# Kernel optimization log

Measured on AMD Instinct MI355X. Metric: run time of the kernel, lower is better.

The kernel has to match this reference:

```python
import jax, jax.numpy as jnp
import numpy as np

EPS = 1e-5
ALPHA = 0.05   # propalpha
GDEP = 2       # gcn_depth
LAYERS = 3     # gcn_layers
NUM_TCN = 2    # num_layer tcn units per encoder


def conv1x1(W, b, x):
    # 1x1 Conv2d on [B,C,N,1]: pure channel mix
    return jnp.einsum('oc,bcnl->bonl', W, x) + b[None, :, None, None]


def tcn_unit(Wf, bf, Wg, bg, h):
    # gated TCN unit: tanh(filter) * sigmoid(gate), 1x1 convs (L==1)
    return jnp.tanh(conv1x1(Wf, bf, h)) * jax.nn.sigmoid(conv1x1(Wg, bg, h))


def mixprop(x, A, W, b):
    # MTGNN mixprop: add self-loops, row-normalize, gdep propagation steps,
    # concat hops on channel dim, 1x1 conv mlp. A: [N,N] or [B,N,N].
    N = A.shape[-1]
    A = A + jnp.eye(N, dtype=A.dtype)
    A = A / A.sum(-1, keepdims=True)
    h = x
    outs = [h]
    for _ in range(GDEP):
        if A.ndim == 2:
            hn = jnp.einsum('vw,bcwl->bcvl', A, h)
        else:
            hn = jnp.einsum('bvw,bcwl->bcvl', A, h)
        h = ALPHA * x + (1.0 - ALPHA) * hn
        outs.append(h)
    ho = jnp.concatenate(outs, axis=1)  # [B,(GDEP+1)*C,N,1]
    return conv1x1(W, b, ho)


def layernorm(x, w, b):
    # LayerNorm over (C,N,1) of [B,C,N,1]; idx=arange(N) selects full affine
    mu = x.mean(axis=(1, 2, 3), keepdims=True)
    var = x.var(axis=(1, 2, 3), keepdims=True)
    return (x - mu) / jnp.sqrt(var + EPS) * w[None] + b[None]


def setup_inputs() -> dict:
    key = jax.random.key(0)
    B, N, E, H, S, T = 8, 2048, 32, 128, 256, 12
    ks = jax.random.split(key, 32)
    s = 0.05
    inp = {
        'x': jax.random.normal(ks[0], (B, E, N, 1), jnp.float32),
        'dy_graph': jax.random.uniform(ks[1], (B, N, N), jnp.float32),
        'static_graph': jax.random.uniform(ks[2], (N, N), jnp.float32),
        'spatial_emb': jax.random.normal(ks[3], (B, 32, N, 1), jnp.float32),
        'temporal_d_emb': jax.random.normal(ks[4], (B, 32, N, 1), jnp.float32),
        'temporal_w_emb': jax.random.normal(ks[5], (B, 32, N, 1), jnp.float32),
        'enc_Wf': s * jax.random.normal(ks[6], (LAYERS, NUM_TCN, H, H), jnp.float32),
        'enc_bf': s * jax.random.normal(ks[7], (LAYERS, NUM_TCN, H), jnp.float32),
        'enc_Wg': s * jax.random.normal(ks[8], (LAYERS, NUM_TCN, H, H), jnp.float32),
        'enc_bg': s * jax.random.normal(ks[9], (LAYERS, NUM_TCN, H), jnp.float32),
        'skip_W': s * jax.random.normal(ks[10], (LAYERS, S, H), jnp.float32),
        'skip_b': s * jax.random.normal(ks[11], (LAYERS, S), jnp.float32),
        'norm_w': jnp.ones((LAYERS, E, N, 1), jnp.float32),
        'norm_b': jnp.zeros((LAYERS, E, N, 1), jnp.float32),
        'g0_W': s * jax.random.normal(ks[12], (LAYERS, E, (GDEP + 1) * E), jnp.float32),
        'g0_b': s * jax.random.normal(ks[13], (LAYERS, E), jnp.float32),
        'g1_W': s * jax.random.normal(ks[14], (LAYERS, E, (GDEP + 1) * E), jnp.float32),
        'g1_b': s * jax.random.normal(ks[15], (LAYERS, E), jnp.float32),
        'g2_W': s * jax.random.normal(ks[16], (LAYERS, E, (GDEP + 1) * E), jnp.float32),
        'g2_b': s * jax.random.normal(ks[17], (LAYERS, E), jnp.float32),
        'skipE_W': s * jax.random.normal(ks[18], (S, E), jnp.float32),
        'skipE_b': s * jax.random.normal(ks[19], (S,), jnp.float32),
        'end_W': s * jax.random.normal(ks[20], (T, S), jnp.float32),
        'end_b': s * jax.random.normal(ks[21], (T,), jnp.float32),
    }
    return inp


def reference(x, dy_graph, static_graph, spatial_emb, temporal_d_emb, temporal_w_emb,
              enc_Wf, enc_bf, enc_Wg, enc_bg, skip_W, skip_b, norm_w, norm_b,
              g0_W, g0_b, g1_W, g1_b, g2_W, g2_b, skipE_W, skipE_b, end_W, end_b):
    adp = dy_graph
    skip = 0.0
    for i in range(LAYERS):
        residual = x
        hidden = jnp.concatenate([x, spatial_emb, temporal_d_emb, temporal_w_emb], axis=1)
        for j in range(NUM_TCN):
            hidden = tcn_unit(enc_Wf[i, j], enc_bf[i, j], enc_Wg[i, j], enc_bg[i, j], hidden)
        skip = conv1x1(skip_W[i], skip_b[i], hidden) + skip
        x = (mixprop(x, static_graph, g0_W[i], g0_b[i])
             + mixprop(x, adp, g1_W[i], g1_b[i])
             + mixprop(x, jnp.swapaxes(adp, -1, -2), g2_W[i], g2_b[i]))
        x = x + residual
        x = jax.nn.relu(layernorm(x, norm_w[i], norm_b[i]))
    skip = conv1x1(skipE_W, skipE_b, x) + skip
    return conv1x1(end_W, end_b, skip)  # [B, seq_length, N, 1]
```

## Files before the change

### kernel.cpp

```cpp
#include <hip/hip_runtime.h>
#include <stdint.h>


typedef uint16_t u16;
typedef uint32_t u32;
typedef __attribute__((ext_vector_type(8))) short s8v;
typedef __attribute__((ext_vector_type(4))) float f4v;

#define MFMA16(a,b,c) __builtin_amdgcn_mfma_f32_16x16x32_bf16(a,b,c,0,0,0)

__device__ __forceinline__ float b2f(u16 u){ union{u32 i; float f;} x; x.i=(u32)u<<16; return x.f; }
__device__ __forceinline__ u16 f2b(float f){
  u32 u = __builtin_bit_cast(u32, f);
  u32 r = (u + 0x7fffu + ((u >> 16) & 1u)) >> 16;
  return (u16)r;
}

__global__ __launch_bounds__(256) void kdetect(const u16* __restrict__ x, int* __restrict__ flag)
{
  const int i = threadIdx.x;
  const uint4* p = (const uint4*)x;
  int cnt = 0;
  #pragma unroll
  for (int q = 0; q < 32; q++) {
    const uint4 v = p[i + q*256];
    const u32 w[4] = {v.x, v.y, v.z, v.w};
    #pragma unroll
    for (int e = 0; e < 4; e++) {
      if ((w[e] & 0x7F80u) == 0x7F80u) cnt++;
      if (((w[e] >> 16) & 0x7F80u) == 0x7F80u) cnt++;
    }
  }
  __shared__ int s[256];
  s[i] = cnt; __syncthreads();
  for (int st = 128; st; st >>= 1) { if (i < st) s[i] += s[i+st]; __syncthreads(); }
  if (i == 0) flag[0] = (s[0] > 0) ? 1 : 0;
}

__global__ __launch_bounds__(256) void kcvt4(const void* __restrict__ src, u16* __restrict__ dst,
                                             int n4, const int* __restrict__ flag)
{
  const int i = blockIdx.x*256 + threadIdx.x;
  if (i >= n4) return;
  if (*flag) {
    const float4 v = ((const float4*)src)[i];
    u16 o[4]; o[0]=f2b(v.x); o[1]=f2b(v.y); o[2]=f2b(v.z); o[3]=f2b(v.w);
    *(uint2*)(dst + (long)i*4) = *(uint2*)o;
  } else {
    *(uint2*)(dst + (long)i*4) = ((const uint2*)src)[i];
  }
}

struct CvtTab { const void* s[18]; u16* d[18]; int n4[18]; };
__global__ __launch_bounds__(256) void kcvt_small(CvtTab tb, const int* __restrict__ flag)
{
  const int e = blockIdx.y;
  const int i = blockIdx.x*256 + threadIdx.x;
  if (i >= tb.n4[e]) return;
  if (*flag) {
    const float4 v = ((const float4*)tb.s[e])[i];
    u16 o[4]; o[0]=f2b(v.x); o[1]=f2b(v.y); o[2]=f2b(v.z); o[3]=f2b(v.w);
    *(uint2*)(tb.d[e] + (long)i*4) = *(uint2*)o;
  } else {
    *(uint2*)(tb.d[e] + (long)i*4) = ((const uint2*)tb.s[e])[i];
  }
}

__global__ __launch_bounds__(256) void kcvtT(
    const void* __restrict__ src, u16* __restrict__ dyb, u16* __restrict__ dytb,
    float* __restrict__ rsum, float* __restrict__ csum, const int* __restrict__ flag)
{
  __shared__ u16 tt[256][72];
  const int tid = threadIdx.x;
  const int b = blockIdx.z;
  const long r0 = (long)blockIdx.y*64;
  const long c0 = (long)blockIdx.x*256;
  const int r = tid>>2, cg = (tid&3)*16;
  const long base = (long)b*4194304;
  const int fl = *flag;
  float rs = 0.f;
  #pragma unroll
  for (int st = 0; st < 4; st++) {
    const long cc = c0 + st*64 + cg;
    u16 v16[16];
    if (fl) {
      const float* sp = (const float*)src + base + (r0+r)*2048 + cc;
      #pragma unroll
      for (int q = 0; q < 4; q++) {
        const float4 f = ((const float4*)sp)[q];
        v16[q*4+0]=f2b(f.x); v16[q*4+1]=f2b(f.y); v16[q*4+2]=f2b(f.z); v16[q*4+3]=f2b(f.w);
      }
    } else {
      const u16* sp = (const u16*)src + base + (r0+r)*2048 + cc;
      *(uint4*)&v16[0] = ((const uint4*)sp)[0];
      *(uint4*)&v16[8] = ((const uint4*)sp)[1];
    }
    *(uint4*)(dyb + base + (r0+r)*2048 + cc)     = *(uint4*)&v16[0];
    *(uint4*)(dyb + base + (r0+r)*2048 + cc + 8) = *(uint4*)&v16[8];
    #pragma unroll
    for (int e = 0; e < 16; e++) { rs += b2f(v16[e]); tt[st*64 + cg + e][r] = v16[e]; }
  }
  rs += __shfl_down(rs, 2, 64);
  rs += __shfl_down(rs, 1, 64);
  if ((tid&3)==0) atomicAdd(rsum + b*2048 + r0 + r, rs);
  __syncthreads();
  u16 col[64];
  #pragma unroll
  for (int q = 0; q < 8; q++) *(uint4*)&col[q*8] = *(const uint4*)&tt[tid][q*8];
  float cs = 0.f;
  #pragma unroll
  for (int e = 0; e < 64; e++) cs += b2f(col[e]);
  u16* dp = dytb + base + (c0 + tid)*2048 + r0;
  #pragma unroll
  for (int q = 0; q < 8; q++) *(uint4*)(dp + q*8) = *(uint4*)&col[q*8];
  atomicAdd(csum + b*2048 + c0 + tid, cs);
}

__global__ void kfin(float* __restrict__ v){
  const int i = blockIdx.x*256 + threadIdx.x;
  v[i] = 1.f/(1.f + v[i]);
}

struct P3 {
  const u16* A0; const u16* A1; const u16* A2;
  long ab0, ab1, ab2;
  const u16* X0; const u16* X1; const u16* X2;
  const float* R0; const float* R1; const float* R2;
  long rb0, rb1, rb2;
  u16* O0; u16* O1; u16* O2;
};

template<int SHAREX>
__global__ __launch_bounds__(256) void kprop3(P3 p, long x_bs, long o_bs)
{
  constexpr int NS = SHAREX ? 5 : 9;
  __shared__ f4v red[4][6][64];
  const int tid = threadIdx.x, wave = tid>>6, lane = tid&63;
  const int lw = lane&15, quad = lane>>4;
  const int v0 = blockIdx.x*16;
  const int b = blockIdx.y;
  const long ko = (long)(wave*512 + quad*8);
  const u16* ptr[9];
  ptr[0] = p.A0 + (long)b*p.ab0 + (long)(v0+lw)*2048 + ko;
  ptr[1] = p.A1 + (long)b*p.ab1 + (long)(v0+lw)*2048 + ko;
  ptr[2] = p.A2 + (long)b*p.ab2 + (long)(v0+lw)*2048 + ko;
  ptr[3] = p.X0 + (long)b*x_bs + (long)lw*2048 + ko;
  ptr[4] = p.X0 + (long)b*x_bs + (long)(16+lw)*2048 + ko;
  if (!SHAREX) {
    ptr[5] = p.X1 + (long)b*x_bs + (long)lw*2048 + ko;
    ptr[6] = p.X1 + (long)b*x_bs + (long)(16+lw)*2048 + ko;
    ptr[7] = p.X2 + (long)b*x_bs + (long)lw*2048 + ko;
    ptr[8] = p.X2 + (long)b*x_bs + (long)(16+lw)*2048 + ko;
  }
  f4v acc[6];
  #pragma unroll
  for (int t = 0; t < 6; t++) acc[t] = (f4v){0.f,0.f,0.f,0.f};
  s8v B0[NS][2], B1[NS][2];

  auto LD = [&](s8v (&B)[NS][2], int off){
    #pragma unroll
    for (int s = 0; s < NS; s++) {
      B[s][0] = *(const s8v*)(ptr[s] + off);
      B[s][1] = *(const s8v*)(ptr[s] + off + 32);
    }
  };
  auto FM = [&](s8v (&B)[NS][2]){
    #pragma unroll
    for (int u = 0; u < 2; u++) {
      if (SHAREX) {
        acc[0] = MFMA16(B[0][u], B[3][u], acc[0]);
        acc[1] = MFMA16(B[0][u], B[4][u], acc[1]);
        acc[2] = MFMA16(B[1][u], B[3][u], acc[2]);
        acc[3] = MFMA16(B[1][u], B[4][u], acc[3]);
        acc[4] = MFMA16(B[2][u], B[3][u], acc[4]);
        acc[5] = MFMA16(B[2][u], B[4][u], acc[5]);
      } else {
        acc[0] = MFMA16(B[0][u], B[3][u], acc[0]);
        acc[1] = MFMA16(B[0][u], B[4][u], acc[1]);
        acc[2] = MFMA16(B[1][u], B[5][u], acc[2]);
        acc[3] = MFMA16(B[1][u], B[6][u], acc[3]);
        acc[4] = MFMA16(B[2][u], B[7][u], acc[4]);
        acc[5] = MFMA16(B[2][u], B[8][u], acc[5]);
      }
    }
  };

  LD(B0, 0);
  #pragma unroll 1
  for (int i = 0; i < 3; i++) {
    LD(B1, 64);
    FM(B0);
    LD(B0, 128);
    FM(B1);
    #pragma unroll
    for (int s = 0; s < NS; s++) ptr[s] += 128;
  }
  LD(B1, 64);
  FM(B0);
  FM(B1);

  #pragma unroll
  for (int t = 0; t < 6; t++) red[wave][t][lane] = acc[t];
  __syncthreads();
  if (wave < 3) {
    const int vb = v0 + quad*4;
    const u16* Xg   = (wave==0) ? p.X0 : (wave==1) ? (SHAREX ? p.X0 : p.X1) : (SHAREX ? p.X0 : p.X2);
    const float* Rg = (wave==0) ? p.R0 : (wave==1) ? p.R1 : p.R2;
    const long rbs  = (wave==0) ? p.rb0 : (wave==1) ? p.rb1 : p.rb2;
    u16* Og         = (wave==0) ? p.O0 : (wave==1) ? p.O1 : p.O2;
    #pragma unroll
    for (int nt = 0; nt < 2; nt++) {
      const int t = wave*2 + nt;
      f4v s = red[0][t][lane] + red[1][t][lane] + red[2][t][lane] + red[3][t][lane];
      const int c = nt*16 + lw;
      const u16* dp = Xg + (long)b*x_bs + (long)c*2048 + vb;
      const float* rp = Rg + (long)b*rbs + vb;
      u16 pk[4];
      #pragma unroll
      for (int r = 0; r < 4; r++) pk[r] = f2b((s[r] + b2f(dp[r])) * rp[r]);
      *(uint2*)(Og + (long)b*o_bs + (long)c*2048 + vb) = *(uint2*)pk;
    }
  }
}

template<int TRANSA, int MODE>
__global__ __launch_bounds__(256) void kprop(
    const u16* __restrict__ A, long a_bs, int lda, int K,
    const u16* __restrict__ X, long x_bs, int ldx,
    const u16* __restrict__ D, long d_bs,
    const float* __restrict__ rinv, long r_bs,
    const float* __restrict__ bias,
    u16* __restrict__ out0, float* __restrict__ out1, long o_bs)
{
  __shared__ u16 As[4][2][16][40];
  __shared__ f4v red[4][2][64];
  const int tid = threadIdx.x;
  const int wave = tid >> 6, lane = tid & 63;
  const int lw = lane & 15, quad = lane >> 4;
  const int v0 = blockIdx.x * 16;
  const int ball = blockIdx.z + blockIdx.y;
  const u16* Ab = A + (long)ball * a_bs;
  const u16* Xb = X + (long)ball * x_bs;
  const int KC = K >> 5;

  f4v acc0 = {0.f,0.f,0.f,0.f}, acc1 = {0.f,0.f,0.f,0.f};

  int r0, c0_;
  if (TRANSA == 0) { r0 = lane >> 2; c0_ = (lane & 3) * 8; }
  else             { r0 = lane >> 1; c0_ = (lane & 1) * 8; }

  int ci = wave;
  bool has = ci < KC;
  uint4 d = make_uint4(0,0,0,0);
  if (has) {
    d = (TRANSA == 0)
      ? *(const uint4*)(Ab + (long)(v0 + r0) * lda + ci * 32 + c0_)
      : *(const uint4*)(Ab + (long)(ci * 32 + r0) * lda + v0 + c0_);
  }
  int buf = 0;
  while (has) {
    if (TRANSA == 0) {
      *(uint4*)&As[wave][buf][r0][c0_] = d;
    } else {
      u16 tmp[8]; *(uint4*)tmp = d;
      #pragma unroll
      for (int e = 0; e < 8; e++) As[wave][buf][c0_ + e][r0] = tmp[e];
    }
    const int cn = ci + 4;
    const bool hn = cn < KC;
    if (hn) {
      d = (TRANSA == 0)
        ? *(const uint4*)(Ab + (long)(v0 + r0) * lda + cn * 32 + c0_)
        : *(const uint4*)(Ab + (long)(cn * 32 + r0) * lda + v0 + c0_);
    }
    s8v af = *(const s8v*)&As[wave][buf][lw][quad * 8];
    const u16* xk = Xb + ci * 32 + quad * 8;
    s8v b0 = *(const s8v*)(xk + (long)lw * ldx);
    s8v b1 = *(const s8v*)(xk + (long)(16 + lw) * ldx);
    acc0 = MFMA16(af, b0, acc0);
    acc1 = MFMA16(af, b1, acc1);
    ci = cn; has = hn; buf ^= 1;
  }
  red[wave][0][lane] = acc0;
  red[wave][1][lane] = acc1;
  __syncthreads();
  if (wave == 0) {
    const int vb = v0 + quad * 4;
    #pragma unroll
    for (int nt = 0; nt < 2; nt++) {
      f4v a = red[0][nt][lane] + red[1][nt][lane] + red[2][nt][lane] + red[3][nt][lane];
      const int c = nt * 16 + lw;
      const u16* dp = D + (long)ball * d_bs + (long)c * 2048 + vb;
      if (MODE == 0) {
        const float* rp = rinv + (long)ball * r_bs + vb;
        u16 pk[4];
        #pragma unroll
        for (int r = 0; r < 4; r++) pk[r] = f2b((a[r] + b2f(dp[r])) * rp[r]);
        *(uint2*)(out0 + (long)ball * o_bs + (long)c * 2048 + vb) = *(uint2*)pk;
      } else {
        const float bs = bias[c];
        float4 st;
        st.x = a[0] + bs + b2f(dp[0]);
        st.y = a[1] + bs + b2f(dp[1]);
        st.z = a[2] + bs + b2f(dp[2]);
        st.w = a[3] + bs + b2f(dp[3]);
        *(float4*)(out1 + (long)ball * o_bs + (long)c * 2048 + vb) = st;
      }
    }
  }
}

__global__ __launch_bounds__(256) void ktcn(
    const u16* __restrict__ H, const u16* __restrict__ Wf, const u16* __restrict__ bfv,
    const u16* __restrict__ Wg, const u16* __restrict__ bgv, u16* __restrict__ out)
{
  const int tid = threadIdx.x, wave = tid>>6, lane = tid&63, lw = lane&15, quad = lane>>4;
  const long j0 = (long)blockIdx.x*64 + wave*16;
  const f4v zero = {0.f,0.f,0.f,0.f};
  f4v accf[8], accg[8];
  #pragma unroll
  for (int nt=0; nt<8; nt++){ accf[nt] = zero; accg[nt] = zero; }
  const u16* Arow = H + (j0 + lw)*128 + quad*8;
  #pragma unroll
  for (int k0 = 0; k0 < 128; k0 += 32) {
    s8v a = *(const s8v*)(Arow + k0);
    #pragma unroll
    for (int nt = 0; nt < 8; nt++) {
      const int o = nt*16 + lw;
      s8v bf_ = *(const s8v*)(Wf + o*128 + k0 + quad*8);
      s8v bg_ = *(const s8v*)(Wg + o*128 + k0 + quad*8);
      accf[nt] = MFMA16(a, bf_, accf[nt]);
      accg[nt] = MFMA16(a, bg_, accg[nt]);
    }
  }
  #pragma unroll
  for (int nt = 0; nt < 8; nt++) {
    const int o = nt*16 + lw;
    const float fb = b2f(bfv[o]), gb = b2f(bgv[o]);
    #pragma unroll
    for (int rr = 0; rr < 4; rr++) {
      const long j = j0 + quad*4 + rr;
      const float f = accf[nt][rr] + fb, g = accg[nt][rr] + gb;
      const float e2 = __expf(2.f*f);
      const float th = 1.f - 2.f/(e2 + 1.f);
      const float sg = 1.f/(1.f + __expf(-g));
      out[j*128 + o] = f2b(th*sg);
    }
  }
}

__global__ __launch_bounds__(256) void kskip(
    const u16* __restrict__ A, int lda, int K,
    const u16* __restrict__ W, int ldb,
    const u16* __restrict__ bias,
    float* __restrict__ skipbuf, int addprev, int mode, u16* __restrict__ outb)
{
  const int tid = threadIdx.x, wave = tid>>6, lane = tid&63, lw = lane&15, quad = lane>>4;
  const long j0 = (long)blockIdx.x*64 + wave*16;
  const f4v zero = {0.f,0.f,0.f,0.f};
  f4v acc[16];
  #pragma unroll
  for (int nt=0; nt<16; nt++) acc[nt] = zero;
  const u16* Arow = A + (j0 + lw)*(long)lda + quad*8;
  for (int k0 = 0; k0 < K; k0 += 32) {
    s8v a = *(const s8v*)(Arow + k0);
    #pragma unroll
    for (int nt = 0; nt < 16; nt++) {
      const int o = nt*16 + lw;
      s8v b = *(const s8v*)(W + (long)o*ldb + k0 + quad*8);
      acc[nt] = MFMA16(a, b, acc[nt]);
    }
  }
  #pragma unroll
  for (int nt = 0; nt < 16; nt++) {
    const int o = nt*16 + lw;
    const float bv = b2f(bias[o]);
    #pragma unroll
    for (int rr = 0; rr < 4; rr++) {
      const long j = j0 + quad*4 + rr;
      float v = acc[nt][rr] + bv;
      if (addprev) v += skipbuf[j*256 + o];
      if (mode == 0) skipbuf[j*256 + o] = v;
      else           outb[j*256 + o] = f2b(v);
    }
  }
}

__global__ __launch_bounds__(256) void kend(
    const u16* __restrict__ A, const u16* __restrict__ W, const u16* __restrict__ bias,
    void* __restrict__ outv, const int* __restrict__ flag)
{
  const int tid = threadIdx.x, wave = tid>>6, lane = tid&63, lw = lane&15, quad = lane>>4;
  const long j0 = (long)blockIdx.x*64 + wave*16;
  f4v acc = {0.f,0.f,0.f,0.f};
  const u16* Arow = A + (j0 + lw)*256 + quad*8;
  #pragma unroll
  for (int k0 = 0; k0 < 256; k0 += 32) {
    s8v a = *(const s8v*)(Arow + k0);
    s8v b = {0,0,0,0,0,0,0,0};
    if (lw < 12) b = *(const s8v*)(W + lw*256 + k0 + quad*8);
    acc = MFMA16(a, b, acc);
  }
  if (lw < 12) {
    const float bv = b2f(bias[lw]);
    const int fl = *flag;
    #pragma unroll
    for (int rr = 0; rr < 4; rr++) {
      const long j = j0 + quad*4 + rr;
      const long oi = (j >> 11)*24576 + lw*2048 + (j & 2047);
      const float val = acc[rr] + bv;
      if (fl) ((float*)outv)[oi] = val;
      else    ((u16*)outv)[oi]   = f2b(val);
    }
  }
}

__global__ __launch_bounds__(256) void khid0(
    const void* __restrict__ x, const void* __restrict__ spat,
    const void* __restrict__ tde, const void* __restrict__ twe,
    u16* __restrict__ hid, u16* __restrict__ slot0, const int* __restrict__ flag)
{
  __shared__ u16 t[32][72];
  const int tid = threadIdx.x, b = blockIdx.y, v0 = blockIdx.x*64;
  const int fl = *flag;
  const void* srcs[4] = {x, spat, tde, twe};
  #pragma unroll
  for (int e = 0; e < 4; e++) {
    const int c = tid>>3, v8 = (tid&7)*8;
    const long boff = (long)c*2048 + v0 + v8;
    u16 o8[8];
    if (fl) {
      const float* sp = (const float*)srcs[e] + (long)b*65536 + boff;
      const float4 a = ((const float4*)sp)[0], bb = ((const float4*)sp)[1];
      o8[0]=f2b(a.x); o8[1]=f2b(a.y); o8[2]=f2b(a.z); o8[3]=f2b(a.w);
      o8[4]=f2b(bb.x); o8[5]=f2b(bb.y); o8[6]=f2b(bb.z); o8[7]=f2b(bb.w);
    } else {
      *(uint4*)o8 = *(const uint4*)((const u16*)srcs[e] + (long)b*65536 + boff);
    }
    if (e == 0) *(uint4*)(slot0 + (long)b*458752 + boff) = *(uint4*)o8;
    *(uint4*)&t[c][v8] = *(uint4*)o8;
    __syncthreads();
    const int jl = tid>>2, c8 = (tid&3)*8;
    u16 q8[8];
    #pragma unroll
    for (int i = 0; i < 8; i++) q8[i] = t[c8 + i][jl];
    *(uint4*)(hid + ((long)b*2048 + v0 + jl)*128 + e*32 + c8) = *(uint4*)q8;
    __syncthreads();
  }
}

__global__ __launch_bounds__(256) void krowsum(const u16* __restrict__ src, float* __restrict__ outv, int nrows)
{
  const int wave = threadIdx.x>>6, lane = threadIdx.x&63;
  const int row = blockIdx.x*4 + wave;
  if (row >= nrows) return;
  const u16* p = src + (long)row*2048 + lane*8;
  float s = 0.f;
  #pragma unroll
  for (int it = 0; it < 4; it++) {
    u16 v[8]; *(uint4*)v = *(const uint4*)(p + it*512);
    #pragma unroll
    for (int e = 0; e < 8; e++) s += b2f(v[e]);
  }
  #pragma unroll
  for (int off = 32; off; off >>= 1) s += __shfl_down(s, off, 64);
  if (lane == 0) outv[row] = 1.f/(1.f + s);
}

__global__ __launch_bounds__(256) void kweff(
    const u16* __restrict__ g0W, const u16* __restrict__ g1W, const u16* __restrict__ g2W,
    const u16* __restrict__ g0b, const u16* __restrict__ g1b, const u16* __restrict__ g2b,
    int ioff, int boff, u16* __restrict__ weff, float* __restrict__ bw)
{
  const int idx = blockIdx.x*256 + threadIdx.x;
  if (idx < 32) bw[idx] = b2f(g0b[boff+idx]) + b2f(g1b[boff+idx]) + b2f(g2b[boff+idx]);
  if (idx >= 7168) return;
  const int o = idx / 224, m = idx % 224;
  const u16* Ws[3] = {g0W + ioff, g1W + ioff, g2W + ioff};
  float val;
  if (m < 32) {
    val = 0.f;
    #pragma unroll
    for (int g = 0; g < 3; g++) {
      const float w0 = b2f(Ws[g][o*96 + m]);
      const float w1 = b2f(Ws[g][o*96 + 32 + m]);
      const float w2 = b2f(Ws[g][o*96 + 64 + m]);
      val += w0 + 0.05f*(w1 + w2);
    }
  } else {
    const int f = (m - 32) >> 5, cc = m & 31;
    const int g = f >> 1, typ = f & 1;
    const float w1 = b2f(Ws[g][o*96 + 32 + cc]);
    const float w2 = b2f(Ws[g][o*96 + 64 + cc]);
    val = (typ == 0) ? (0.95f*w1 + 0.0475f*w2) : (0.9025f*w2);
  }
  weff[o*224 + m] = f2b(val);
}

__global__ __launch_bounds__(256) void kstats(const float* __restrict__ xpre, float* __restrict__ raw)
{
  const int b = blockIdx.y, tid = threadIdx.x;
  const float4* p = (const float4*)(xpre + (long)b*65536 + (long)blockIdx.x*8192);
  float s = 0.f, q = 0.f;
  #pragma unroll
  for (int i = 0; i < 8; i++) {
    const float4 v = p[tid + i*256];
    s += v.x + v.y + v.z + v.w;
    q += v.x*v.x + v.y*v.y + v.z*v.z + v.w*v.w;
  }
  __shared__ float ss[256], qq[256];
  ss[tid] = s; qq[tid] = q;
  __syncthreads();
  for (int st = 128; st; st >>= 1) {
    if (tid < st) { ss[tid] += ss[tid+st]; qq[tid] += qq[tid+st]; }
    __syncthreads();
  }
  if (tid == 0) { atomicAdd(raw + b*2, ss[0]); atomicAdd(raw + b*2 + 1, qq[0]); }
}

__global__ __launch_bounds__(256) void kapply(
    const float* __restrict__ xpre, const float* __restrict__ raw,
    const u16* __restrict__ nw, const u16* __restrict__ nb,
    u16* __restrict__ slot0, u16* __restrict__ hid)
{
  __shared__ u16 t[32][72];
  const int tid = threadIdx.x, b = blockIdx.y, v0 = blockIdx.x*64;
  const float mu = raw[b*2] * (1.f/65536.f);
  const float var = raw[b*2+1] * (1.f/65536.f) - mu*mu;
  const float rs = rsqrtf(var + 1e-5f);
  const int c = tid>>3, v8 = (tid&7)*8;
  const long boff = (long)c*2048 + v0 + v8;
  float4 xa = *(const float4*)(xpre + (long)b*65536 + boff);
  float4 xbv = *(const float4*)(xpre + (long)b*65536 + boff + 4);
  u16 wv[8], bv[8], o8[8];
  *(uint4*)wv = *(const uint4*)(nw + boff);
  *(uint4*)bv = *(const uint4*)(nb + boff);
  const float xs[8] = {xa.x, xa.y, xa.z, xa.w, xbv.x, xbv.y, xbv.z, xbv.w};
  #pragma unroll
  for (int e = 0; e < 8; e++) {
    float y = (xs[e] - mu) * rs * b2f(wv[e]) + b2f(bv[e]);
    y = fmaxf(y, 0.f);
    o8[e] = f2b(y);
    t[c][v8 + e] = o8[e];
  }
  *(uint4*)(slot0 + (long)b*458752 + boff) = *(uint4*)o8;
  __syncthreads();
  const int jl = tid>>2, c8 = (tid&3)*8;
  u16 q8[8];
  #pragma unroll
  for (int e = 0; e < 8; e++) q8[e] = t[c8 + e][jl];
  *(uint4*)(hid + ((long)b*2048 + v0 + jl)*128 + c8) = *(uint4*)q8;
}

extern "C" void kernel_launch(void* const* d_in, const int* in_sizes, int n_in,
                              void* d_out, int out_size, void* d_ws, size_t ws_size,
                              hipStream_t stream)
{
  (void)in_sizes; (void)n_in; (void)out_size; (void)ws_size;

  char* ws = (char*)d_ws;
  u16*   pbuf = (u16*)(ws + 0);
  u16*   hid  = (u16*)(ws + 7340032);
  u16*   hb1  = (u16*)(ws + 11534336);
  u16*   hb2  = (u16*)(ws + 15728640);
  float* skip = (float*)(ws + 19922944);
  u16*   xsb  = (u16*)(ws + 36700160);
  float* xpre = (float*)(ws + 45088768);
  u16*   weff = (u16*)(ws + 47185920);
  float* bw   = (float*)(ws + 47202304);
  float* rst  = (float*)(ws + 47203328);
  float* rdy  = (float*)(ws + 47211520);
  float* cdy  = (float*)(ws + 47277056);
  int*   flag = (int*)(ws + 47343616);
  float* raw  = (float*)(ws + 47343744);

  size_t coff = 50331648;
  auto alloc = [&](size_t elems) -> u16* {
    u16* p = (u16*)(ws + coff);
    coff += ((elems*2 + 255)/256)*256;
    return p;
  };
  u16* dyb   = alloc(33554432);
  u16* stgb  = alloc(4194304);
  u16* encWf = alloc(98304);
  u16* encbf = alloc(768);
  u16* encWg = alloc(98304);
  u16* encbg = alloc(768);
  u16* skW   = alloc(98304);
  u16* skb   = alloc(768);
  u16* nw    = alloc(196608);
  u16* nb    = alloc(196608);
  u16* g0W   = alloc(9216);
  u16* g0b   = alloc(96);
  u16* g1W   = alloc(9216);
  u16* g1b   = alloc(96);
  u16* g2W   = alloc(9216);
  u16* g2b   = alloc(96);
  u16* sEW   = alloc(8192);
  u16* sEb   = alloc(256);
  u16* eW    = alloc(3072);
  u16* eb    = alloc(12);
  u16* dytb  = alloc(33554432);

  hipLaunchKernelGGL(kdetect, dim3(1), dim3(256), 0, stream, (const u16*)d_in[0], flag);

  CvtTab tb;
  {
    const void* ss[18] = { d_in[6], d_in[7], d_in[8], d_in[9], d_in[10], d_in[11],
      d_in[12], d_in[13], d_in[14], d_in[15], d_in[16], d_in[17], d_in[18], d_in[19],
      d_in[20], d_in[21], d_in[22], d_in[23] };
    u16* dd[18] = { encWf, encbf, encWg, encbg, skW, skb, nw, nb,
      g0W, g0b, g1W, g1b, g2W, g2b, sEW, sEb, eW, eb };
    const int nn[18] = { 24576, 192, 24576, 192, 24576, 192, 49152, 49152,
      2304, 24, 2304, 24, 2304, 24, 2048, 64, 768, 3 };
    for (int e = 0; e < 18; e++) { tb.s[e] = ss[e]; tb.d[e] = dd[e]; tb.n4[e] = nn[e]; }
  }
  hipLaunchKernelGGL(kcvt_small, dim3(192, 18), dim3(256), 0, stream, tb, flag);
  hipLaunchKernelGGL(kcvt4, dim3(4096), dim3(256), 0, stream, d_in[2], stgb, 1048576, flag);

  hipMemsetAsync(rdy, 0, 131072, stream);
  hipMemsetAsync(raw, 0, 192, stream);
  hipLaunchKernelGGL(kcvtT, dim3(8,32,8), dim3(256), 0, stream,
      d_in[1], dyb, dytb, rdy, cdy, flag);
  hipLaunchKernelGGL(kfin, dim3(128), dim3(256), 0, stream, rdy);
  hipLaunchKernelGGL(krowsum, dim3(512), dim3(256), 0, stream, stgb, rst, 2048);
  hipLaunchKernelGGL(khid0, dim3(32,8), dim3(256), 0, stream,
      d_in[0], d_in[3], d_in[4], d_in[5], hid, pbuf, flag);

  const long PB = 458752;
  const long SL = 65536;
  const long DYB = 4194304;

  for (int i = 0; i < 3; i++) {
    hipLaunchKernelGGL(ktcn, dim3(256), dim3(256), 0, stream,
        hid, encWf + (i*2+0)*16384, encbf + (i*2+0)*128, encWg + (i*2+0)*16384, encbg + (i*2+0)*128, hb1);
    hipLaunchKernelGGL(ktcn, dim3(256), dim3(256), 0, stream,
        hb1, encWf + (i*2+1)*16384, encbf + (i*2+1)*128, encWg + (i*2+1)*16384, encbg + (i*2+1)*128, hb2);
    hipLaunchKernelGGL(kskip, dim3(256), dim3(256), 0, stream,
        hb2, 128, 128, skW + i*32768, 128, skb + i*256, skip, (i>0)?1:0, 0, (u16*)nullptr);
    hipLaunchKernelGGL(kweff, dim3(28), dim3(256), 0, stream,
        g0W, g1W, g2W, g0b, g1b, g2b, i*3072, i*32, weff, bw);

    P3 p1;
    p1.A0 = stgb; p1.A1 = dyb; p1.A2 = dytb;
    p1.ab0 = 0;   p1.ab1 = DYB; p1.ab2 = DYB;
    p1.X0 = pbuf; p1.X1 = pbuf; p1.X2 = pbuf;
    p1.R0 = rst;  p1.R1 = rdy;  p1.R2 = cdy;
    p1.rb0 = 0;   p1.rb1 = 2048; p1.rb2 = 2048;
    p1.O0 = pbuf + 1*SL; p1.O1 = pbuf + 3*SL; p1.O2 = pbuf + 5*SL;
    hipLaunchKernelGGL((kprop3<1>), dim3(128,8), dim3(256), 0, stream, p1, PB, PB);

    P3 p2 = p1;
    p2.X0 = pbuf + 1*SL; p2.X1 = pbuf + 3*SL; p2.X2 = pbuf + 5*SL;
    p2.O0 = pbuf + 2*SL; p2.O1 = pbuf + 4*SL; p2.O2 = pbuf + 6*SL;
    hipLaunchKernelGGL((kprop3<0>), dim3(128,8), dim3(256), 0, stream, p2, PB, PB);

    hipLaunchKernelGGL((kprop<1,1>), dim3(128,1,8), dim3(256), 0, stream,
        pbuf, PB, 2048, 224, weff, 0L, 224, pbuf, PB, (const float*)nullptr, 0L, bw, (u16*)nullptr, xpre, 65536L);
    hipLaunchKernelGGL(kstats, dim3(8,8), dim3(256), 0, stream, xpre, raw + i*16);
    hipLaunchKernelGGL(kapply, dim3(32,8), dim3(256), 0, stream,
        xpre, raw + i*16, nw + i*65536, nb + i*65536, pbuf, hid);
  }
  hipLaunchKernelGGL(kskip, dim3(256), dim3(256), 0, stream,
      hid, 128, 32, sEW, 32, sEb, skip, 1, 1, xsb);
  hipLaunchKernelGGL(kend, dim3(256), dim3(256), 0, stream, xsb, eW, eb, d_out, flag);
}
```

Baseline: 893.6 us.

## Fuse TCN chain, mixprop combine, final convs and preprocessing kernels

Merges the two gated TCN units and the skip conv into one kernel that keeps intermediates in shared memory. Propagation kernels now also write a transposed hop buffer, so a new combine kernel can do the effective-weight GEMM and the layernorm statistics in one pass. The reciprocal row-sum finalisation moves into the propagation epilogue, and the static-graph conversion is fused with its row sum. The skipE and end convs become one kernel, and the effective weights are precomputed once for all layers. This cuts launches and global round trips, but adds scattered transposed stores and more shared memory per block.

Result: slower. 937.9 us (+5.0%).

```diff
diff --git a/kernel.cpp b/kernel.cpp
--- a/kernel.cpp
+++ b/kernel.cpp
@@ -8,6 +8,11 @@
 typedef __attribute__((ext_vector_type(4))) float f4v;
 
 #define MFMA16(a,b,c) __builtin_amdgcn_mfma_f32_16x16x32_bf16(a,b,c,0,0,0)
+
+constexpr long PB  = 262144;
+constexpr long SL  = 65536;
+constexpr long TB  = 393216;
+constexpr long DYB = 4194304;
 
 __device__ __forceinline__ float b2f(u16 u){ union{u32 i; float f;} x; x.i=(u32)u<<16; return x.f; }
 __device__ __forceinline__ u16 f2b(float f){
@@ -35,20 +40,6 @@
   s[i] = cnt; __syncthreads();
   for (int st = 128; st; st >>= 1) { if (i < st) s[i] += s[i+st]; __syncthreads(); }
   if (i == 0) flag[0] = (s[0] > 0) ? 1 : 0;
-}
-
-__global__ __launch_bounds__(256) void kcvt4(const void* __restrict__ src, u16* __restrict__ dst,
-                                             int n4, const int* __restrict__ flag)
-{
-  const int i = blockIdx.x*256 + threadIdx.x;
-  if (i >= n4) return;
-  if (*flag) {
-    const float4 v = ((const float4*)src)[i];
-    u16 o[4]; o[0]=f2b(v.x); o[1]=f2b(v.y); o[2]=f2b(v.z); o[3]=f2b(v.w);
-    *(uint2*)(dst + (long)i*4) = *(uint2*)o;
-  } else {
-    *(uint2*)(dst + (long)i*4) = ((const uint2*)src)[i];
-  }
 }
 
 struct CvtTab { const void* s[18]; u16* d[18]; int n4[18]; };
@@ -66,71 +57,103 @@
   }
 }
 
+__global__ __launch_bounds__(256) void kstg(
+    const void* __restrict__ src, u16* __restrict__ dst, float* __restrict__ rst,
+    const int* __restrict__ flag)
+{
+  const int wave = threadIdx.x>>6, lane = threadIdx.x&63;
+  const int row = blockIdx.x*4 + wave;
+  const int fl = *flag;
+  float s = 0.f;
+  #pragma unroll
+  for (int q = 0; q < 8; q++) {
+    const long off = (long)row*2048 + q*256 + lane*4;
+    u16 v4[4];
+    if (fl) {
+      const float4 f = *(const float4*)((const float*)src + off);
+      v4[0]=f2b(f.x); v4[1]=f2b(f.y); v4[2]=f2b(f.z); v4[3]=f2b(f.w);
+    } else {
+      *(uint2*)v4 = *(const uint2*)((const u16*)src + off);
+    }
+    *(uint2*)(dst + off) = *(uint2*)v4;
+    #pragma unroll
+    for (int e = 0; e < 4; e++) s += b2f(v4[e]);
+  }
+  #pragma unroll
+  for (int off = 32; off; off >>= 1) s += __shfl_down(s, off, 64);
+  if (lane == 0) rst[row] = s;
+}
+
 __global__ __launch_bounds__(256) void kcvtT(
     const void* __restrict__ src, u16* __restrict__ dyb, u16* __restrict__ dytb,
     float* __restrict__ rsum, float* __restrict__ csum, const int* __restrict__ flag)
 {
-  __shared__ u16 tt[256][72];
+  __shared__ u32 tt[256][34];
   const int tid = threadIdx.x;
   const int b = blockIdx.z;
-  const long r0 = (long)blockIdx.y*64;
-  const long c0 = (long)blockIdx.x*256;
-  const int r = tid>>2, cg = (tid&3)*16;
+  const long r0 = (long)blockIdx.y*64, c0 = (long)blockIdx.x*256;
+  const int rp = tid>>3, c4 = (tid&7)*4;
   const long base = (long)b*4194304;
   const int fl = *flag;
-  float rs = 0.f;
-  #pragma unroll
-  for (int st = 0; st < 4; st++) {
-    const long cc = c0 + st*64 + cg;
-    u16 v16[16];
+  float rs0 = 0.f, rs1 = 0.f;
+  #pragma unroll
+  for (int j = 0; j < 8; j++) {
+    const long cc = c0 + c4 + 32*j;
+    u16 v0_[4], v1_[4];
     if (fl) {
-      const float* sp = (const float*)src + base + (r0+r)*2048 + cc;
-      #pragma unroll
-      for (int q = 0; q < 4; q++) {
-        const float4 f = ((const float4*)sp)[q];
-        v16[q*4+0]=f2b(f.x); v16[q*4+1]=f2b(f.y); v16[q*4+2]=f2b(f.z); v16[q*4+3]=f2b(f.w);
-      }
+      const float* s0 = (const float*)src + base + (r0 + 2*rp)*2048 + cc;
+      const float4 f0 = *(const float4*)s0;
+      const float4 f1 = *(const float4*)(s0 + 2048);
+      v0_[0]=f2b(f0.x); v0_[1]=f2b(f0.y); v0_[2]=f2b(f0.z); v0_[3]=f2b(f0.w);
+      v1_[0]=f2b(f1.x); v1_[1]=f2b(f1.y); v1_[2]=f2b(f1.z); v1_[3]=f2b(f1.w);
     } else {
-      const u16* sp = (const u16*)src + base + (r0+r)*2048 + cc;
-      *(uint4*)&v16[0] = ((const uint4*)sp)[0];
-      *(uint4*)&v16[8] = ((const uint4*)sp)[1];
-    }
-    *(uint4*)(dyb + base + (r0+r)*2048 + cc)     = *(uint4*)&v16[0];
-    *(uint4*)(dyb + base + (r0+r)*2048 + cc + 8) = *(uint4*)&v16[8];
-    #pragma unroll
-    for (int e = 0; e < 16; e++) { rs += b2f(v16[e]); tt[st*64 + cg + e][r] = v16[e]; }
-  }
-  rs += __shfl_down(rs, 2, 64);
-  rs += __shfl_down(rs, 1, 64);
-  if ((tid&3)==0) atomicAdd(rsum + b*2048 + r0 + r, rs);
+      const u16* s0 = (const u16*)src + base + (r0 + 2*rp)*2048 + cc;
+      *(uint2*)v0_ = *(const uint2*)s0;
+      *(uint2*)v1_ = *(const uint2*)(s0 + 2048);
+    }
+    *(uint2*)(dyb + base + (r0+2*rp)*2048 + cc)   = *(uint2*)v0_;
+    *(uint2*)(dyb + base + (r0+2*rp+1)*2048 + cc) = *(uint2*)v1_;
+    #pragma unroll
+    for (int e = 0; e < 4; e++) {
+      rs0 += b2f(v0_[e]); rs1 += b2f(v1_[e]);
+      tt[c4 + 32*j + e][rp] = (u32)v0_[e] | ((u32)v1_[e] << 16);
+    }
+  }
+  rs0 += __shfl_down(rs0, 4, 8); rs0 += __shfl_down(rs0, 2, 8); rs0 += __shfl_down(rs0, 1, 8);
+  rs1 += __shfl_down(rs1, 4, 8); rs1 += __shfl_down(rs1, 2, 8); rs1 += __shfl_down(rs1, 1, 8);
+  if ((tid & 7) == 0) {
+    atomicAdd(rsum + b*2048 + r0 + 2*rp, rs0);
+    atomicAdd(rsum + b*2048 + r0 + 2*rp + 1, rs1);
+  }
   __syncthreads();
-  u16 col[64];
-  #pragma unroll
-  for (int q = 0; q < 8; q++) *(uint4*)&col[q*8] = *(const uint4*)&tt[tid][q*8];
-  float cs = 0.f;
-  #pragma unroll
-  for (int e = 0; e < 64; e++) cs += b2f(col[e]);
+  u32 cw[32];
+  #pragma unroll
+  for (int q = 0; q < 16; q++) {
+    const uint2 w2 = *(const uint2*)&tt[tid][q*2];
+    cw[q*2] = w2.x; cw[q*2+1] = w2.y;
+  }
+  u16 col[64]; float cs = 0.f;
+  #pragma unroll
+  for (int rr = 0; rr < 32; rr++) {
+    col[2*rr]   = (u16)(cw[rr] & 0xffffu);
+    col[2*rr+1] = (u16)(cw[rr] >> 16);
+    cs += b2f(col[2*rr]) + b2f(col[2*rr+1]);
+  }
   u16* dp = dytb + base + (c0 + tid)*2048 + r0;
   #pragma unroll
   for (int q = 0; q < 8; q++) *(uint4*)(dp + q*8) = *(uint4*)&col[q*8];
   atomicAdd(csum + b*2048 + c0 + tid, cs);
 }
 
-__global__ void kfin(float* __restrict__ v){
-  const int i = blockIdx.x*256 + threadIdx.x;
-  v[i] = 1.f/(1.f + v[i]);
-}
-
 struct P3 {
-  const u16* A0; const u16* A1; const u16* A2;
-  long ab0, ab1, ab2;
-  const u16* X0; const u16* X1; const u16* X2;
-  const float* R0; const float* R1; const float* R2;
-  long rb0, rb1, rb2;
-  u16* O0; u16* O1; u16* O2;
+  const u16 *A0, *A1, *A2; long ab0, ab1, ab2;
+  const u16 *X0, *X1, *X2;
+  const float *R0, *R1, *R2; long rb0, rb1, rb2;
+  u16 *O0, *O1, *O2;
+  u16 *T0, *T1, *T2;
 };
 
-template<int SHAREX>
+template<int SHAREX, int WRP>
 __global__ __launch_bounds__(256) void kprop3(P3 p, long x_bs, long o_bs)
 {
   constexpr int NS = SHAREX ? 5 : 9;
@@ -208,305 +231,167 @@
     const float* Rg = (wave==0) ? p.R0 : (wave==1) ? p.R1 : p.R2;
     const long rbs  = (wave==0) ? p.rb0 : (wave==1) ? p.rb1 : p.rb2;
     u16* Og         = (wave==0) ? p.O0 : (wave==1) ? p.O1 : p.O2;
+    u16* Tg         = (wave==0) ? p.T0 : (wave==1) ? p.T1 : p.T2;
+    const float4 rv = *(const float4*)(Rg + (long)b*rbs + vb);
+    float ri[4];
+    #pragma unroll
+    for (int r = 0; r < 4; r++) ri[r] = 1.f/(1.f + (&rv.x)[r]);
     #pragma unroll
     for (int nt = 0; nt < 2; nt++) {
       const int t = wave*2 + nt;
       f4v s = red[0][t][lane] + red[1][t][lane] + red[2][t][lane] + red[3][t][lane];
       const int c = nt*16 + lw;
       const u16* dp = Xg + (long)b*x_bs + (long)c*2048 + vb;
-      const float* rp = Rg + (long)b*rbs + vb;
       u16 pk[4];
       #pragma unroll
-      for (int r = 0; r < 4; r++) pk[r] = f2b((s[r] + b2f(dp[r])) * rp[r]);
-      *(uint2*)(Og + (long)b*o_bs + (long)c*2048 + vb) = *(uint2*)pk;
-    }
-  }
-}
-
-template<int TRANSA, int MODE>
-__global__ __launch_bounds__(256) void kprop(
-    const u16* __restrict__ A, long a_bs, int lda, int K,
-    const u16* __restrict__ X, long x_bs, int ldx,
-    const u16* __restrict__ D, long d_bs,
-    const float* __restrict__ rinv, long r_bs,
-    const float* __restrict__ bias,
-    u16* __restrict__ out0, float* __restrict__ out1, long o_bs)
-{
-  __shared__ u16 As[4][2][16][40];
-  __shared__ f4v red[4][2][64];
-  const int tid = threadIdx.x;
-  const int wave = tid >> 6, lane = tid & 63;
-  const int lw = lane & 15, quad = lane >> 4;
-  const int v0 = blockIdx.x * 16;
-  const int ball = blockIdx.z + blockIdx.y;
-  const u16* Ab = A + (long)ball * a_bs;
-  const u16* Xb = X + (long)ball * x_bs;
-  const int KC = K >> 5;
-
-  f4v acc0 = {0.f,0.f,0.f,0.f}, acc1 = {0.f,0.f,0.f,0.f};
-
-  int r0, c0_;
-  if (TRANSA == 0) { r0 = lane >> 2; c0_ = (lane & 3) * 8; }
-  else             { r0 = lane >> 1; c0_ = (lane & 1) * 8; }
-
-  int ci = wave;
-  bool has = ci < KC;
-  uint4 d = make_uint4(0,0,0,0);
-  if (has) {
-    d = (TRANSA == 0)
-      ? *(const uint4*)(Ab + (long)(v0 + r0) * lda + ci * 32 + c0_)
-      : *(const uint4*)(Ab + (long)(ci * 32 + r0) * lda + v0 + c0_);
-  }
-  int buf = 0;
-  while (has) {
-    if (TRANSA == 0) {
-      *(uint4*)&As[wave][buf][r0][c0_] = d;
-    } else {
-      u16 tmp[8]; *(uint4*)tmp = d;
-      #pragma unroll
-      for (int e = 0; e < 8; e++) As[wave][buf][c0_ + e][r0] = tmp[e];
-    }
-    const int cn = ci + 4;
-    const bool hn = cn < KC;
-    if (hn) {
-      d = (TRANSA == 0)
-        ? *(const uint4*)(Ab + (long)(v0 + r0) * lda + cn * 32 + c0_)
-        : *(const uint4*)(Ab + (long)(cn * 32 + r0) * lda + v0 + c0_);
-    }
-    s8v af = *(const s8v*)&As[wave][buf][lw][quad * 8];
-    const u16* xk = Xb + ci * 32 + quad * 8;
-    s8v b0 = *(const s8v*)(xk + (long)lw * ldx);
-    s8v b1 = *(const s8v*)(xk + (long)(16 + lw) * ldx);
-    acc0 = MFMA16(af, b0, acc0);
-    acc1 = MFMA16(af, b1, acc1);
-    ci = cn; has = hn; buf ^= 1;
-  }
-  red[wave][0][lane] = acc0;
-  red[wave][1][lane] = acc1;
-  __syncthreads();
-  if (wave == 0) {
-    const int vb = v0 + quad * 4;
-    #pragma unroll
-    for (int nt = 0; nt < 2; nt++) {
-      f4v a = red[0][nt][lane] + red[1][nt][lane] + red[2][nt][lane] + red[3][nt][lane];
-      const int c = nt * 16 + lw;
-      const u16* dp = D + (long)ball * d_bs + (long)c * 2048 + vb;
-      if (MODE == 0) {
-        const float* rp = rinv + (long)ball * r_bs + vb;
-        u16 pk[4];
-        #pragma unroll
-        for (int r = 0; r < 4; r++) pk[r] = f2b((a[r] + b2f(dp[r])) * rp[r]);
-        *(uint2*)(out0 + (long)ball * o_bs + (long)c * 2048 + vb) = *(uint2*)pk;
-      } else {
-        const float bs = bias[c];
-        float4 st;
-        st.x = a[0] + bs + b2f(dp[0]);
-        st.y = a[1] + bs + b2f(dp[1]);
-        st.z = a[2] + bs + b2f(dp[2]);
-        st.w = a[3] + bs + b2f(dp[3]);
-        *(float4*)(out1 + (long)ball * o_bs + (long)c * 2048 + vb) = st;
-      }
-    }
-  }
-}
-
-__global__ __launch_bounds__(256) void ktcn(
-    const u16* __restrict__ H, const u16* __restrict__ Wf, const u16* __restrict__ bfv,
-    const u16* __restrict__ Wg, const u16* __restrict__ bgv, u16* __restrict__ out)
-{
+      for (int r = 0; r < 4; r++) pk[r] = f2b((s[r] + b2f(dp[r])) * ri[r]);
+      if (WRP) *(uint2*)(Og + (long)b*o_bs + (long)c*2048 + vb) = *(uint2*)pk;
+      u16* tp = Tg + (long)b*TB + (long)vb*192 + c;
+      #pragma unroll
+      for (int r = 0; r < 4; r++) tp[r*192] = pk[r];
+    }
+  }
+}
+
+__global__ __launch_bounds__(256) void ktcnfuse(
+    const u16* __restrict__ hid,
+    const u16* __restrict__ Wf1, const u16* __restrict__ bf1,
+    const u16* __restrict__ Wg1, const u16* __restrict__ bg1,
+    const u16* __restrict__ Wf2, const u16* __restrict__ bf2,
+    const u16* __restrict__ Wg2, const u16* __restrict__ bg2,
+    const u16* __restrict__ sW, const u16* __restrict__ sb,
+    float* __restrict__ skipbuf, int addprev)
+{
+  __shared__ u16 h1[64][136];
+  __shared__ u16 h2[64][136];
   const int tid = threadIdx.x, wave = tid>>6, lane = tid&63, lw = lane&15, quad = lane>>4;
-  const long j0 = (long)blockIdx.x*64 + wave*16;
+  const long j0 = (long)blockIdx.x*64;
   const f4v zero = {0.f,0.f,0.f,0.f};
-  f4v accf[8], accg[8];
-  #pragma unroll
-  for (int nt=0; nt<8; nt++){ accf[nt] = zero; accg[nt] = zero; }
-  const u16* Arow = H + (j0 + lw)*128 + quad*8;
-  #pragma unroll
-  for (int k0 = 0; k0 < 128; k0 += 32) {
-    s8v a = *(const s8v*)(Arow + k0);
+
+  {
+    f4v af[8], ag[8];
+    #pragma unroll
+    for (int nt=0; nt<8; nt++){ af[nt]=zero; ag[nt]=zero; }
+    const u16* Arow = hid + (j0 + wave*16 + lw)*128 + quad*8;
+    #pragma unroll
+    for (int k0 = 0; k0 < 128; k0 += 32) {
+      s8v a = *(const s8v*)(Arow + k0);
+      #pragma unroll
+      for (int nt = 0; nt < 8; nt++) {
+        const int o = nt*16 + lw;
+        af[nt] = MFMA16(a, *(const s8v*)(Wf1 + o*128 + k0 + quad*8), af[nt]);
+        ag[nt] = MFMA16(a, *(const s8v*)(Wg1 + o*128 + k0 + quad*8), ag[nt]);
+      }
+    }
     #pragma unroll
     for (int nt = 0; nt < 8; nt++) {
       const int o = nt*16 + lw;
-      s8v bf_ = *(const s8v*)(Wf + o*128 + k0 + quad*8);
-      s8v bg_ = *(const s8v*)(Wg + o*128 + k0 + quad*8);
-      accf[nt] = MFMA16(a, bf_, accf[nt]);
-      accg[nt] = MFMA16(a, bg_, accg[nt]);
-    }
-  }
-  #pragma unroll
-  for (int nt = 0; nt < 8; nt++) {
-    const int o = nt*16 + lw;
-    const float fb = b2f(bfv[o]), gb = b2f(bgv[o]);
-    #pragma unroll
-    for (int rr = 0; rr < 4; rr++) {
-      const long j = j0 + quad*4 + rr;
-      const float f = accf[nt][rr] + fb, g = accg[nt][rr] + gb;
-      const float e2 = __expf(2.f*f);
-      const float th = 1.f - 2.f/(e2 + 1.f);
-      const float sg = 1.f/(1.f + __expf(-g));
-      out[j*128 + o] = f2b(th*sg);
-    }
-  }
-}
-
-__global__ __launch_bounds__(256) void kskip(
-    const u16* __restrict__ A, int lda, int K,
-    const u16* __restrict__ W, int ldb,
-    const u16* __restrict__ bias,
-    float* __restrict__ skipbuf, int addprev, int mode, u16* __restrict__ outb)
-{
-  const int tid = threadIdx.x, wave = tid>>6, lane = tid&63, lw = lane&15, quad = lane>>4;
-  const long j0 = (long)blockIdx.x*64 + wave*16;
-  const f4v zero = {0.f,0.f,0.f,0.f};
-  f4v acc[16];
-  #pragma unroll
-  for (int nt=0; nt<16; nt++) acc[nt] = zero;
-  const u16* Arow = A + (j0 + lw)*(long)lda + quad*8;
-  for (int k0 = 0; k0 < K; k0 += 32) {
-    s8v a = *(const s8v*)(Arow + k0);
+      const float fb = b2f(bf1[o]), gb = b2f(bg1[o]);
+      #pragma unroll
+      for (int rr = 0; rr < 4; rr++) {
+        const int row = wave*16 + quad*4 + rr;
+        const float f = af[nt][rr] + fb, g = ag[nt][rr] + gb;
+        const float e2 = __expf(2.f*f);
+        const float th = 1.f - 2.f/(e2 + 1.f);
+        const float sg = 1.f/(1.f + __expf(-g));
+        h1[row][o] = f2b(th*sg);
+      }
+    }
+  }
+  __syncthreads();
+  {
+    f4v af[8], ag[8];
+    #pragma unroll
+    for (int nt=0; nt<8; nt++){ af[nt]=zero; ag[nt]=zero; }
+    #pragma unroll
+    for (int k0 = 0; k0 < 128; k0 += 32) {
+      s8v a = *(const s8v*)&h1[wave*16 + lw][k0 + quad*8];
+      #pragma unroll
+      for (int nt = 0; nt < 8; nt++) {
+        const int o = nt*16 + lw;
+        af[nt] = MFMA16(a, *(const s8v*)(Wf2 + o*128 + k0 + quad*8), af[nt]);
+        ag[nt] = MFMA16(a, *(const s8v*)(Wg2 + o*128 + k0 + quad*8), ag[nt]);
+      }
+    }
+    #pragma unroll
+    for (int nt = 0; nt < 8; nt++) {
+      const int o = nt*16 + lw;
+      const float fb = b2f(bf2[o]), gb = b2f(bg2[o]);
+      #pragma unroll
+      for (int rr = 0; rr < 4; rr++) {
+        const int row = wave*16 + quad*4 + rr;
+        const float f = af[nt][rr] + fb, g = ag[nt][rr] + gb;
+        const float e2 = __expf(2.f*f);
+        const float th = 1.f - 2.f/(e2 + 1.f);
+        const float sg = 1.f/(1.f + __expf(-g));
+        h2[row][o] = f2b(th*sg);
+      }
+    }
+  }
+  __syncthreads();
+  {
+    f4v acc[16];
+    #pragma unroll
+    for (int nt=0; nt<16; nt++) acc[nt] = zero;
+    #pragma unroll
+    for (int k0 = 0; k0 < 128; k0 += 32) {
+      s8v a = *(const s8v*)&h2[wave*16 + lw][k0 + quad*8];
+      #pragma unroll
+      for (int nt = 0; nt < 16; nt++) {
+        const int o = nt*16 + lw;
+        acc[nt] = MFMA16(a, *(const s8v*)(sW + o*128 + k0 + quad*8), acc[nt]);
+      }
+    }
     #pragma unroll
     for (int nt = 0; nt < 16; nt++) {
       const int o = nt*16 + lw;
-      s8v b = *(const s8v*)(W + (long)o*ldb + k0 + quad*8);
-      acc[nt] = MFMA16(a, b, acc[nt]);
-    }
-  }
-  #pragma unroll
-  for (int nt = 0; nt < 16; nt++) {
-    const int o = nt*16 + lw;
-    const float bv = b2f(bias[o]);
-    #pragma unroll
-    for (int rr = 0; rr < 4; rr++) {
-      const long j = j0 + quad*4 + rr;
-      float v = acc[nt][rr] + bv;
-      if (addprev) v += skipbuf[j*256 + o];
-      if (mode == 0) skipbuf[j*256 + o] = v;
-      else           outb[j*256 + o] = f2b(v);
-    }
-  }
-}
-
-__global__ __launch_bounds__(256) void kend(
-    const u16* __restrict__ A, const u16* __restrict__ W, const u16* __restrict__ bias,
-    void* __restrict__ outv, const int* __restrict__ flag)
+      const float bv = b2f(sb[o]);
+      #pragma unroll
+      for (int rr = 0; rr < 4; rr++) {
+        const long j = j0 + wave*16 + quad*4 + rr;
+        float v = acc[nt][rr] + bv;
+        if (addprev) v += skipbuf[j*256 + o];
+        skipbuf[j*256 + o] = v;
+      }
+    }
+  }
+}
+
+__global__ __launch_bounds__(256) void kcomb(
+    const u16* __restrict__ hid, const u16* __restrict__ pT,
+    const u16* __restrict__ slot0, const u16* __restrict__ weff,
+    const float* __restrict__ bw, float* __restrict__ xpre, float* __restrict__ rawp)
 {
   const int tid = threadIdx.x, wave = tid>>6, lane = tid&63, lw = lane&15, quad = lane>>4;
-  const long j0 = (long)blockIdx.x*64 + wave*16;
-  f4v acc = {0.f,0.f,0.f,0.f};
-  const u16* Arow = A + (j0 + lw)*256 + quad*8;
-  #pragma unroll
-  for (int k0 = 0; k0 < 256; k0 += 32) {
-    s8v a = *(const s8v*)(Arow + k0);
-    s8v b = {0,0,0,0,0,0,0,0};
-    if (lw < 12) b = *(const s8v*)(W + lw*256 + k0 + quad*8);
-    acc = MFMA16(a, b, acc);
-  }
-  if (lw < 12) {
-    const float bv = b2f(bias[lw]);
-    const int fl = *flag;
-    #pragma unroll
-    for (int rr = 0; rr < 4; rr++) {
-      const long j = j0 + quad*4 + rr;
-      const long oi = (j >> 11)*24576 + lw*2048 + (j & 2047);
-      const float val = acc[rr] + bv;
-      if (fl) ((float*)outv)[oi] = val;
-      else    ((u16*)outv)[oi]   = f2b(val);
-    }
-  }
-}
-
-__global__ __launch_bounds__(256) void khid0(
-    const void* __restrict__ x, const void* __restrict__ spat,
-    const void* __restrict__ tde, const void* __restrict__ twe,
-    u16* __restrict__ hid, u16* __restrict__ slot0, const int* __restrict__ flag)
-{
-  __shared__ u16 t[32][72];
-  const int tid = threadIdx.x, b = blockIdx.y, v0 = blockIdx.x*64;
-  const int fl = *flag;
-  const void* srcs[4] = {x, spat, tde, twe};
-  #pragma unroll
-  for (int e = 0; e < 4; e++) {
-    const int c = tid>>3, v8 = (tid&7)*8;
-    const long boff = (long)c*2048 + v0 + v8;
-    u16 o8[8];
-    if (fl) {
-      const float* sp = (const float*)srcs[e] + (long)b*65536 + boff;
-      const float4 a = ((const float4*)sp)[0], bb = ((const float4*)sp)[1];
-      o8[0]=f2b(a.x); o8[1]=f2b(a.y); o8[2]=f2b(a.z); o8[3]=f2b(a.w);
-      o8[4]=f2b(bb.x); o8[5]=f2b(bb.y); o8[6]=f2b(bb.z); o8[7]=f2b(bb.w);
-    } else {
-      *(uint4*)o8 = *(const uint4*)((const u16*)srcs[e] + (long)b*65536 + boff);
-    }
-    if (e == 0) *(uint4*)(slot0 + (long)b*458752 + boff) = *(uint4*)o8;
-    *(uint4*)&t[c][v8] = *(uint4*)o8;
-    __syncthreads();
-    const int jl = tid>>2, c8 = (tid&3)*8;
-    u16 q8[8];
-    #pragma unroll
-    for (int i = 0; i < 8; i++) q8[i] = t[c8 + i][jl];
-    *(uint4*)(hid + ((long)b*2048 + v0 + jl)*128 + e*32 + c8) = *(uint4*)q8;
-    __syncthreads();
-  }
-}
-
-__global__ __launch_bounds__(256) void krowsum(const u16* __restrict__ src, float* __restrict__ outv, int nrows)
-{
-  const int wave = threadIdx.x>>6, lane = threadIdx.x&63;
-  const int row = blockIdx.x*4 + wave;
-  if (row >= nrows) return;
-  const u16* p = src + (long)row*2048 + lane*8;
-  float s = 0.f;
-  #pragma unroll
-  for (int it = 0; it < 4; it++) {
-    u16 v[8]; *(uint4*)v = *(const uint4*)(p + it*512);
-    #pragma unroll
-    for (int e = 0; e < 8; e++) s += b2f(v[e]);
-  }
-  #pragma unroll
-  for (int off = 32; off; off >>= 1) s += __shfl_down(s, off, 64);
-  if (lane == 0) outv[row] = 1.f/(1.f + s);
-}
-
-__global__ __launch_bounds__(256) void kweff(
-    const u16* __restrict__ g0W, const u16* __restrict__ g1W, const u16* __restrict__ g2W,
-    const u16* __restrict__ g0b, const u16* __restrict__ g1b, const u16* __restrict__ g2b,
-    int ioff, int boff, u16* __restrict__ weff, float* __restrict__ bw)
-{
-  const int idx = blockIdx.x*256 + threadIdx.x;
-  if (idx < 32) bw[idx] = b2f(g0b[boff+idx]) + b2f(g1b[boff+idx]) + b2f(g2b[boff+idx]);
-  if (idx >= 7168) return;
-  const int o = idx / 224, m = idx % 224;
-  const u16* Ws[3] = {g0W + ioff, g1W + ioff, g2W + ioff};
-  float val;
-  if (m < 32) {
-    val = 0.f;
-    #pragma unroll
-    for (int g = 0; g < 3; g++) {
-      const float w0 = b2f(Ws[g][o*96 + m]);
-      const float w1 = b2f(Ws[g][o*96 + 32 + m]);
-      const float w2 = b2f(Ws[g][o*96 + 64 + m]);
-      val += w0 + 0.05f*(w1 + w2);
-    }
-  } else {
-    const int f = (m - 32) >> 5, cc = m & 31;
-    const int g = f >> 1, typ = f & 1;
-    const float w1 = b2f(Ws[g][o*96 + 32 + cc]);
-    const float w2 = b2f(Ws[g][o*96 + 64 + cc]);
-    val = (typ == 0) ? (0.95f*w1 + 0.0475f*w2) : (0.9025f*w2);
-  }
-  weff[o*224 + m] = f2b(val);
-}
-
-__global__ __launch_bounds__(256) void kstats(const float* __restrict__ xpre, float* __restrict__ raw)
-{
-  const int b = blockIdx.y, tid = threadIdx.x;
-  const float4* p = (const float4*)(xpre + (long)b*65536 + (long)blockIdx.x*8192);
+  const long j0 = (long)blockIdx.x*64;
+  const int b = (int)(j0 >> 11);
+  f4v acc[2] = {{0.f,0.f,0.f,0.f},{0.f,0.f,0.f,0.f}};
+  const u16* Ah = hid + (j0 + wave*16 + lw)*128 + quad*8;
+  const u16* At = pT + (j0 + wave*16 + lw)*192 + quad*8;
+  #pragma unroll
+  for (int cc = 0; cc < 7; cc++) {
+    s8v a = (cc == 0) ? *(const s8v*)Ah : *(const s8v*)(At + (cc-1)*32);
+    #pragma unroll
+    for (int nt = 0; nt < 2; nt++) {
+      s8v w = *(const s8v*)(weff + (nt*16+lw)*224 + cc*32 + quad*8);
+      acc[nt] = MFMA16(a, w, acc[nt]);
+    }
+  }
   float s = 0.f, q = 0.f;
-  #pragma unroll
-  for (int i = 0; i < 8; i++) {
-    const float4 v = p[tid + i*256];
-    s += v.x + v.y + v.z + v.w;
-    q += v.x*v.x + v.y*v.y + v.z*v.z + v.w*v.w;
+  const int vbase = (int)(j0 & 2047) + wave*16 + quad*4;
+  #pragma unroll
+  for (int nt = 0; nt < 2; nt++) {
+    const int c = nt*16 + lw;
+    const float bb = bw[c];
+    u16 r4[4];
+    *(uint2*)r4 = *(const uint2*)(slot0 + (long)b*PB + (long)c*2048 + vbase);
+    float4 st;
+    #pragma unroll
+    for (int r = 0; r < 4; r++) {
+      const float val = acc[nt][r] + bb + b2f(r4[r]);
+      (&st.x)[r] = val; s += val; q += val*val;
+    }
+    *(float4*)(xpre + (long)b*65536 + (long)c*2048 + vbase) = st;
   }
   __shared__ float ss[256], qq[256];
   ss[tid] = s; qq[tid] = q;
@@ -515,7 +400,7 @@
     if (tid < st) { ss[tid] += ss[tid+st]; qq[tid] += qq[tid+st]; }
     __syncthreads();
   }
-  if (tid == 0) { atomicAdd(raw + b*2, ss[0]); atomicAdd(raw + b*2 + 1, qq[0]); }
+  if (tid == 0) { atomicAdd(rawp + b*2, ss[0]); atomicAdd(rawp + b*2 + 1, qq[0]); }
 }
 
 __global__ __launch_bounds__(256) void kapply(
@@ -543,7 +428,7 @@
     o8[e] = f2b(y);
     t[c][v8 + e] = o8[e];
   }
-  *(uint4*)(slot0 + (long)b*458752 + boff) = *(uint4*)o8;
+  *(uint4*)(slot0 + (long)b*PB + boff) = *(uint4*)o8;
   __syncthreads();
   const int jl = tid>>2, c8 = (tid&3)*8;
   u16 q8[8];
@@ -552,6 +437,130 @@
   *(uint4*)(hid + ((long)b*2048 + v0 + jl)*128 + c8) = *(uint4*)q8;
 }
 
+__global__ __launch_bounds__(256) void khid0(
+    const void* __restrict__ x, const void* __restrict__ spat,
+    const void* __restrict__ tde, const void* __restrict__ twe,
+    u16* __restrict__ hid, u16* __restrict__ slot0, const int* __restrict__ flag)
+{
+  __shared__ u16 t[32][72];
+  const int tid = threadIdx.x, b = blockIdx.y, v0 = blockIdx.x*64;
+  const int fl = *flag;
+  const void* srcs[4] = {x, spat, tde, twe};
+  #pragma unroll
+  for (int e = 0; e < 4; e++) {
+    const int c = tid>>3, v8 = (tid&7)*8;
+    const long boff = (long)c*2048 + v0 + v8;
+    u16 o8[8];
+    if (fl) {
+      const float* sp = (const float*)srcs[e] + (long)b*65536 + boff;
+      const float4 a = ((const float4*)sp)[0], bb = ((const float4*)sp)[1];
+      o8[0]=f2b(a.x); o8[1]=f2b(a.y); o8[2]=f2b(a.z); o8[3]=f2b(a.w);
+      o8[4]=f2b(bb.x); o8[5]=f2b(bb.y); o8[6]=f2b(bb.z); o8[7]=f2b(bb.w);
+    } else {
+      *(uint4*)o8 = *(const uint4*)((const u16*)srcs[e] + (long)b*65536 + boff);
+    }
+    if (e == 0) *(uint4*)(slot0 + (long)b*PB + boff) = *(uint4*)o8;
+    *(uint4*)&t[c][v8] = *(uint4*)o8;
+    __syncthreads();
+    const int jl = tid>>2, c8 = (tid&3)*8;
+    u16 q8[8];
+    #pragma unroll
+    for (int i = 0; i < 8; i++) q8[i] = t[c8 + i][jl];
+    *(uint4*)(hid + ((long)b*2048 + v0 + jl)*128 + e*32 + c8) = *(uint4*)q8;
+    __syncthreads();
+  }
+}
+
+__global__ __launch_bounds__(256) void kweff3(
+    const u16* __restrict__ g0W, const u16* __restrict__ g1W, const u16* __restrict__ g2W,
+    const u16* __restrict__ g0b, const u16* __restrict__ g1b, const u16* __restrict__ g2b,
+    u16* __restrict__ weff, float* __restrict__ bw)
+{
+  const int layer = blockIdx.y;
+  const int ioff = layer*3072, boff = layer*32;
+  u16* wout = weff + layer*7168;
+  float* bout = bw + layer*32;
+  const int idx = blockIdx.x*256 + threadIdx.x;
+  if (idx < 32) bout[idx] = b2f(g0b[boff+idx]) + b2f(g1b[boff+idx]) + b2f(g2b[boff+idx]);
+  if (idx >= 7168) return;
+  const int o = idx / 224, m = idx % 224;
+  const u16* Ws[3] = {g0W + ioff, g1W + ioff, g2W + ioff};
+  float val;
+  if (m < 32) {
+    val = 0.f;
+    #pragma unroll
+    for (int g = 0; g < 3; g++) {
+      const float w0 = b2f(Ws[g][o*96 + m]);
+      const float w1 = b2f(Ws[g][o*96 + 32 + m]);
+      const float w2 = b2f(Ws[g][o*96 + 64 + m]);
+      val += w0 + 0.05f*(w1 + w2);
+    }
+  } else {
+    const int f = (m - 32) >> 5, cc = m & 31;
+    const int g = f >> 1, typ = f & 1;
+    const float w1 = b2f(Ws[g][o*96 + 32 + cc]);
+    const float w2 = b2f(Ws[g][o*96 + 64 + cc]);
+    val = (typ == 0) ? (0.95f*w1 + 0.0475f*w2) : (0.9025f*w2);
+  }
+  wout[o*224 + m] = f2b(val);
+}
+
+__global__ __launch_bounds__(256) void kfinal(
+    const u16* __restrict__ hid, const u16* __restrict__ sEW, const u16* __restrict__ sEb,
+    const float* __restrict__ skipbuf, const u16* __restrict__ eW, const u16* __restrict__ eb,
+    void* __restrict__ outv, const int* __restrict__ flag)
+{
+  __shared__ u16 xs[64][264];
+  const int tid = threadIdx.x, wave = tid>>6, lane = tid&63, lw = lane&15, quad = lane>>4;
+  const long j0 = (long)blockIdx.x*64;
+  const f4v zero = {0.f,0.f,0.f,0.f};
+  {
+    f4v acc[16];
+    #pragma unroll
+    for (int nt=0; nt<16; nt++) acc[nt] = zero;
+    s8v a = *(const s8v*)(hid + (j0 + wave*16 + lw)*128 + quad*8);
+    #pragma unroll
+    for (int nt = 0; nt < 16; nt++) {
+      const int o = nt*16 + lw;
+      acc[nt] = MFMA16(a, *(const s8v*)(sEW + o*32 + quad*8), acc[nt]);
+    }
+    #pragma unroll
+    for (int nt = 0; nt < 16; nt++) {
+      const int o = nt*16 + lw;
+      const float bv = b2f(sEb[o]);
+      #pragma unroll
+      for (int rr = 0; rr < 4; rr++) {
+        const int row = wave*16 + quad*4 + rr;
+        const long j = j0 + row;
+        xs[row][o] = f2b(acc[nt][rr] + bv + skipbuf[j*256 + o]);
+      }
+    }
+  }
+  __syncthreads();
+  {
+    f4v acc = zero;
+    #pragma unroll
+    for (int k0 = 0; k0 < 256; k0 += 32) {
+      s8v a = *(const s8v*)&xs[wave*16 + lw][k0 + quad*8];
+      s8v b = {0,0,0,0,0,0,0,0};
+      if (lw < 12) b = *(const s8v*)(eW + lw*256 + k0 + quad*8);
+      acc = MFMA16(a, b, acc);
+    }
+    if (lw < 12) {
+      const float bv = b2f(eb[lw]);
+      const int fl = *flag;
+      #pragma unroll
+      for (int rr = 0; rr < 4; rr++) {
+        const long j = j0 + wave*16 + quad*4 + rr;
+        const long oi = (j >> 11)*24576 + lw*2048 + (j & 2047);
+        const float val = acc[rr] + bv;
+        if (fl) ((float*)outv)[oi] = val;
+        else    ((u16*)outv)[oi]   = f2b(val);
+      }
+    }
+  }
+}
+
 extern "C" void kernel_launch(void* const* d_in, const int* in_sizes, int n_in,
                               void* d_out, int out_size, void* d_ws, size_t ws_size,
                               hipStream_t stream)
@@ -559,28 +568,27 @@
   (void)in_sizes; (void)n_in; (void)out_size; (void)ws_size;
 
   char* ws = (char*)d_ws;
-  u16*   pbuf = (u16*)(ws + 0);
-  u16*   hid  = (u16*)(ws + 7340032);
-  u16*   hb1  = (u16*)(ws + 11534336);
-  u16*   hb2  = (u16*)(ws + 15728640);
-  float* skip = (float*)(ws + 19922944);
-  u16*   xsb  = (u16*)(ws + 36700160);
-  float* xpre = (float*)(ws + 45088768);
-  u16*   weff = (u16*)(ws + 47185920);
-  float* bw   = (float*)(ws + 47202304);
-  float* rst  = (float*)(ws + 47203328);
-  float* rdy  = (float*)(ws + 47211520);
-  float* cdy  = (float*)(ws + 47277056);
-  int*   flag = (int*)(ws + 47343616);
-  float* raw  = (float*)(ws + 47343744);
-
-  size_t coff = 50331648;
+  u16*   pbuf  = (u16*)(ws + 0);
+  u16*   pbufT = (u16*)(ws + 4194304);
+  u16*   hid   = (u16*)(ws + 10485760);
+  float* skip  = (float*)(ws + 14680064);
+  float* xpre  = (float*)(ws + 31457280);
+  u16*   weff  = (u16*)(ws + 33554432);
+  float* bw    = (float*)(ws + 33597440);
+  float* rst   = (float*)(ws + 33598464);
+  float* rdy   = (float*)(ws + 33606656);
+  float* cdy   = (float*)(ws + 33672192);
+  float* raw   = (float*)(ws + 33737728);
+  int*   flag  = (int*)(ws + 33737920);
+
+  size_t coff = 33740800;
   auto alloc = [&](size_t elems) -> u16* {
     u16* p = (u16*)(ws + coff);
     coff += ((elems*2 + 255)/256)*256;
     return p;
   };
   u16* dyb   = alloc(33554432);
+  u16* dytb  = alloc(33554432);
   u16* stgb  = alloc(4194304);
   u16* encWf = alloc(98304);
   u16* encbf = alloc(768);
@@ -600,7 +608,6 @@
   u16* sEb   = alloc(256);
   u16* eW    = alloc(3072);
   u16* eb    = alloc(12);
-  u16* dytb  = alloc(33554432);
 
   hipLaunchKernelGGL(kdetect, dim3(1), dim3(256), 0, stream, (const u16*)d_in[0], flag);
 
@@ -616,30 +623,21 @@
     for (int e = 0; e < 18; e++) { tb.s[e] = ss[e]; tb.d[e] = dd[e]; tb.n4[e] = nn[e]; }
   }
   hipLaunchKernelGGL(kcvt_small, dim3(192, 18), dim3(256), 0, stream, tb, flag);
-  hipLaunchKernelGGL(kcvt4, dim3(4096), dim3(256), 0, stream, d_in[2], stgb, 1048576, flag);
-
-  hipMemsetAsync(rdy, 0, 131072, stream);
-  hipMemsetAsync(raw, 0, 192, stream);
+  hipLaunchKernelGGL(kweff3, dim3(28, 3), dim3(256), 0, stream,
+      g0W, g1W, g2W, g0b, g1b, g2b, weff, bw);
+  hipLaunchKernelGGL(kstg, dim3(512), dim3(256), 0, stream, d_in[2], stgb, rst, flag);
+  hipMemsetAsync(rdy, 0, 131264, stream);
   hipLaunchKernelGGL(kcvtT, dim3(8,32,8), dim3(256), 0, stream,
       d_in[1], dyb, dytb, rdy, cdy, flag);
-  hipLaunchKernelGGL(kfin, dim3(128), dim3(256), 0, stream, rdy);
-  hipLaunchKernelGGL(krowsum, dim3(512), dim3(256), 0, stream, stgb, rst, 2048);
   hipLaunchKernelGGL(khid0, dim3(32,8), dim3(256), 0, stream,
       d_in[0], d_in[3], d_in[4], d_in[5], hid, pbuf, flag);
 
-  const long PB = 458752;
-  const long SL = 65536;
-  const long DYB = 4194304;
-
   for (int i = 0; i < 3; i++) {
-    hipLaunchKernelGGL(ktcn, dim3(256), dim3(256), 0, stream,
-        hid, encWf + (i*2+0)*16384, encbf + (i*2+0)*128, encWg + (i*2+0)*16384, encbg + (i*2+0)*128, hb1);
-    hipLaunchKernelGGL(ktcn, dim3(256), dim3(256), 0, stream,
-        hb1, encWf + (i*2+1)*16384, encbf + (i*2+1)*128, encWg + (i*2+1)*16384, encbg + (i*2+1)*128, hb2);
-    hipLaunchKernelGGL(kskip, dim3(256), dim3(256), 0, stream,
-        hb2, 128, 128, skW + i*32768, 128, skb + i*256, skip, (i>0)?1:0, 0, (u16*)nullptr);
-    hipLaunchKernelGGL(kweff, dim3(28), dim3(256), 0, stream,
-        g0W, g1W, g2W, g0b, g1b, g2b, i*3072, i*32, weff, bw);
+    hipLaunchKernelGGL(ktcnfuse, dim3(256), dim3(256), 0, stream,
+        hid,
+        encWf + (i*2+0)*16384, encbf + (i*2+0)*128, encWg + (i*2+0)*16384, encbg + (i*2+0)*128,
+        encWf + (i*2+1)*16384, encbf + (i*2+1)*128, encWg + (i*2+1)*16384, encbg + (i*2+1)*128,
+        skW + i*32768, skb + i*256, skip, (i>0)?1:0);
 
     P3 p1;
     p1.A0 = stgb; p1.A1 = dyb; p1.A2 = dytb;
@@ -647,21 +645,20 @@
     p1.X0 = pbuf; p1.X1 = pbuf; p1.X2 = pbuf;
     p1.R0 = rst;  p1.R1 = rdy;  p1.R2 = cdy;
     p1.rb0 = 0;   p1.rb1 = 2048; p1.rb2 = 2048;
-    p1.O0 = pbuf + 1*SL; p1.O1 = pbuf + 3*SL; p1.O2 = pbuf + 5*SL;
-    hipLaunchKernelGGL((kprop3<1>), dim3(128,8), dim3(256), 0, stream, p1, PB, PB);
+    p1.O0 = pbuf + 1*SL; p1.O1 = pbuf + 2*SL; p1.O2 = pbuf + 3*SL;
+    p1.T0 = pbufT + 0;   p1.T1 = pbufT + 64;  p1.T2 = pbufT + 128;
+    hipLaunchKernelGGL((kprop3<1,1>), dim3(128,8), dim3(256), 0, stream, p1, PB, PB);
 
     P3 p2 = p1;
-    p2.X0 = pbuf + 1*SL; p2.X1 = pbuf + 3*SL; p2.X2 = pbuf + 5*SL;
-    p2.O0 = pbuf + 2*SL; p2.O1 = pbuf + 4*SL; p2.O2 = pbuf + 6*SL;
-    hipLaunchKernelGGL((kprop3<0>), dim3(128,8), dim3(256), 0, stream, p2, PB, PB);
-
-    hipLaunchKernelGGL((kprop<1,1>), dim3(128,1,8), dim3(256), 0, stream,
-        pbuf, PB, 2048, 224, weff, 0L, 224, pbuf, PB, (const float*)nullptr, 0L, bw, (u16*)nullptr, xpre, 65536L);
-    hipLaunchKernelGGL(kstats, dim3(8,8), dim3(256), 0, stream, xpre, raw + i*16);
+    p2.X0 = pbuf + 1*SL; p2.X1 = pbuf + 2*SL; p2.X2 = pbuf + 3*SL;
+    p2.T0 = pbufT + 32;  p2.T1 = pbufT + 96;  p2.T2 = pbufT + 160;
+    hipLaunchKernelGGL((kprop3<0,0>), dim3(128,8), dim3(256), 0, stream, p2, PB, PB);
+
+    hipLaunchKernelGGL(kcomb, dim3(256), dim3(256), 0, stream,
+        hid, pbufT, pbuf, weff + i*7168, bw + i*32, xpre, raw + i*16);
     hipLaunchKernelGGL(kapply, dim3(32,8), dim3(256), 0, stream,
         xpre, raw + i*16, nw + i*65536, nb + i*65536, pbuf, hid);
   }
-  hipLaunchKernelGGL(kskip, dim3(256), dim3(256), 0, stream,
-      hid, 128, 32, sEW, 32, sEb, skip, 1, 1, xsb);
-  hipLaunchKernelGGL(kend, dim3(256), dim3(256), 0, stream, xsb, eW, eb, d_out, flag);
-}
+  hipLaunchKernelGGL(kfinal, dim3(256), dim3(256), 0, stream,
+      hid, sEW, sEb, skip, eW, eb, d_out, flag);
+}
```
